# Optimization experiments

Measured on AMD Instinct MI355X. Metric: run time of the kernel, lower is better.

## Reference

```python
import jax, jax.numpy as jnp
import numpy as np

B, O, I, D = 8, 128, 128, 1024


def setup_inputs() -> dict:
    key = jax.random.key(0)
    ks = jax.random.split(key, 10)
    s = 1.0 / np.sqrt(2 * D)  # torch Linear default-ish scale
    return {
        "output": jax.random.normal(ks[0], (B, O, D), jnp.float32),
        "context": jax.random.normal(ks[1], (B, I, D), jnp.float32),
        "mask": jax.random.randint(ks[2], (B, I), 0, 2, jnp.int32),
        # self.w = Linear(2*dim, dim), split into the output-half and context-half
        "w_out_w": jax.random.normal(ks[3], (D, D), jnp.float32) * s,
        "w_ctx_w": jax.random.normal(ks[4], (D, D), jnp.float32) * s,
        "w_b": jax.random.normal(ks[5], (D,), jnp.float32) * s,
        # self.score = Linear(dim, 1)
        "score_w": jax.random.normal(ks[6], (D,), jnp.float32) * (1.0 / np.sqrt(D)),
        "score_b": jnp.zeros((), jnp.float32),
        # self.linear_out = Linear(2*dim, dim)
        "lin_w": jax.random.normal(ks[7], (2 * D, D), jnp.float32) * s,
        "lin_b": jax.random.normal(ks[8], (D,), jnp.float32) * s,
    }


def reference(output, context, mask, w_out_w, w_ctx_w, w_b, score_w, score_b, lin_w, lin_b):
    # Additive (Bahdanau) attention.
    # cat(out, ctx) @ W^T == out @ W1 + ctx @ W2  -> avoid [B,O,I,2D] concat.
    s_out = jnp.einsum('bod,de->boe', output, w_out_w)            # [B,O,D]
    s_ctx = jnp.einsum('bid,de->bie', context, w_ctx_w)           # [B,I,D]
    h = jax.nn.leaky_relu(s_out[:, :, None, :] + s_ctx[:, None, :, :] + w_b)  # [B,O,I,D]
    score = jnp.einsum('boid,d->boi', h, score_w) + score_b       # [B,O,I]
    score = jnp.where(mask[:, None, :] == 1, -jnp.inf, score)
    attn = jax.nn.softmax(score, axis=-1)                         # [B,O,I]
    attn_output = jnp.einsum('boi,bid->bod', attn, context)       # mix=True: bmm
    # fn=True: linear_out on cat(attn_output, output) then leaky_relu
    combined = jnp.concatenate([attn_output, output], axis=-1)    # [B,O,2D]
    attn_output = jax.nn.leaky_relu(combined @ lin_w + lin_b)     # [B,O,D]
    return attn_output, attn
```

## Files before the change

kernel.cpp:

```cpp
#include <hip/hip_runtime.h>

namespace {

constexpr int kB = 8, kO = 128, kI = 128, kD = 1024;
constexpr long kOutAttnOff = (long)kB * kO * kD;

typedef __attribute__((ext_vector_type(8))) short short8;
typedef __attribute__((ext_vector_type(4))) float f32x4;
typedef __attribute__((ext_vector_type(2))) float f32x2;
typedef __attribute__((ext_vector_type(2))) unsigned u32x2;

__device__ __forceinline__ float leaky(float x) { return fmaxf(x, 0.01f * x); }

__device__ __forceinline__ short f2bf(float f) {
    unsigned u = __builtin_bit_cast(unsigned, f);
    u += 0x7FFFu + ((u >> 16) & 1u);
    return (short)(u >> 16);
}
__device__ __forceinline__ float bf2f(short h) {
    return __builtin_bit_cast(float, ((unsigned)(unsigned short)h) << 16);
}
__device__ __forceinline__ void b8tofs(const short8 v, float* f) {
    const unsigned* u = (const unsigned*)&v;
#pragma unroll
    for (int j = 0; j < 4; ++j) {
        f[2 * j]     = __builtin_bit_cast(float, u[j] << 16);
        f[2 * j + 1] = __builtin_bit_cast(float, u[j] & 0xffff0000u);
    }
}
__device__ __forceinline__ void bpair(const short8 a, const short8 b, f32x2* p) {
    float fa[8], fb[8];
    b8tofs(a, fa); b8tofs(b, fb);
#pragma unroll
    for (int j = 0; j < 8; ++j) p[j] = f32x2{fa[j], fb[j]};
}
__device__ __forceinline__ f32x2 vabs2(f32x2 x) {
    u32x2 u = __builtin_bit_cast(u32x2, x);
    u &= 0x7fffffffu;
    return __builtin_bit_cast(f32x2, u);
}

__device__ __forceinline__ void gll16(const void* g, void* l) {
    __builtin_amdgcn_global_load_lds(
        (const __attribute__((address_space(1))) int*)g,
        (__attribute__((address_space(3))) int*)l, 16, 0, 0);
}

__global__ __launch_bounds__(256)
void conv_all(const float* __restrict__ output, const float* __restrict__ context,
              const float* __restrict__ w1, const float* __restrict__ w2,
              const float* __restrict__ lin,
              short* __restrict__ ob16, short* __restrict__ cb16,
              short* __restrict__ w1t, short* __restrict__ w2t,
              short* __restrict__ lint)
{
    __shared__ float T[64][68];
    const int bid = blockIdx.x, tid = threadIdx.x;

    if (bid < 1024) {
        const int idx = bid * 256 + tid;
        const float* src; short* dst; int i;
        if (idx < (1 << 17)) { src = output;  dst = ob16; i = idx; }
        else                 { src = context; dst = cb16; i = idx - (1 << 17); }
        const float4* s4 = (const float4*)src + (long)i * 2;
        const float4 v0 = s4[0], v1 = s4[1];
        short8 r;
        r[0] = f2bf(v0.x); r[1] = f2bf(v0.y); r[2] = f2bf(v0.z); r[3] = f2bf(v0.w);
        r[4] = f2bf(v1.x); r[5] = f2bf(v1.y); r[6] = f2bf(v1.z); r[7] = f2bf(v1.w);
        *(short8*)(dst + (long)i * 8) = r;
        return;
    }

    const int tb = bid - 1024;
    const float* src; short* dst; long C, R; int t2;
    if (tb < 256)      { src = w1;  dst = w1t;  R = 1024; C = 1024; t2 = tb; }
    else if (tb < 512) { src = w2;  dst = w2t;  R = 1024; C = 1024; t2 = tb - 256; }
    else               { src = lin; dst = lint; R = 2048; C = 1024; t2 = tb - 512; }
    const int tr = t2 >> 4, tc = t2 & 15;
    const int r = tid >> 2, q = tid & 3;

    const float* s = src + (long)(tr * 64 + r) * C + tc * 64 + q * 16;
    const float4 a0 = ((const float4*)s)[0];
    const float4 a1 = ((const float4*)s)[1];
    const float4 a2 = ((const float4*)s)[2];
    const float4 a3 = ((const float4*)s)[3];
    *(float4*)&T[r][q * 16 + 0]  = a0;
    *(float4*)&T[r][q * 16 + 4]  = a1;
    *(float4*)&T[r][q * 16 + 8]  = a2;
    *(float4*)&T[r][q * 16 + 12] = a3;
    __syncthreads();

    short8 o0, o1;
#pragma unroll
    for (int j = 0; j < 8; ++j)  o0[j] = f2bf(T[q * 16 + j][r]);
#pragma unroll
    for (int j = 0; j < 8; ++j)  o1[j] = f2bf(T[q * 16 + 8 + j][r]);
    short* dp = dst + (long)(tc * 64 + r) * R + tr * 64 + q * 16;
    *(short8*)dp       = o0;
    *((short8*)dp + 1) = o1;
}

__global__ __launch_bounds__(256)
void mm_jobs(const short* __restrict__ ob16, const short* __restrict__ cb16,
             const short* __restrict__ w1t, const short* __restrict__ w2t,
             const short* __restrict__ lint,
             const float* __restrict__ w_b, const float* __restrict__ lin_b,
             float* __restrict__ s_out, short* __restrict__ s_ctx16,
             float* __restrict__ outlin, short* __restrict__ ctxlin)
{
    __shared__ short As[2][64][64];
    __shared__ short Bs[2][128][64];
    const int tid = threadIdx.x;
    const int t = blockIdx.x;
    const int lane = tid & 63, w = tid >> 6;

    const short *Ap, *Bp;
    int lda, ldb, bm, bn, ldc;
    const float* bias = nullptr;
    float* Cf = nullptr;
    short* Ch = nullptr;

    if (t < 384) {
        const int job = t >> 7, jt = t & 127;
        bm = (jt >> 3) * 64; bn = (jt & 7) * 128;
        lda = 1024; ldc = 1024;
        if (job == 0)      { Ap = ob16; Bp = w1t;         ldb = 1024; bias = w_b;   Cf = s_out;   }
        else if (job == 1) { Ap = cb16; Bp = w2t;         ldb = 1024;               Ch = s_ctx16; }
        else               { Ap = ob16; Bp = lint + 1024; ldb = 2048; bias = lin_b; Cf = outlin;  }
    } else {
        const int tt = t - 384, bz = tt >> 4, tw = tt & 15;
        bm = tw * 64; bn = 0;
        Ap = lint; lda = 2048;
        Bp = cb16 + (long)bz * (kI * kD); ldb = 1024;
        Ch = ctxlin + (long)bz * (kD * kI); ldc = 128;
    }

    const int m0 = (w >> 1) * 32, n0 = (w & 1) * 64;
    const int fr = lane & 15, fcol = lane >> 4, sl = lane & 7;
    const int r8 = lane >> 3;
    const int sw8 = ((lane & 7) ^ r8) * 8;
    const int w16 = w * 16, w32 = w * 32;

    f32x4 acc[2][4] = {};

    auto stage = [&](int buf, int k0) {
        const short* ga = Ap + (long)(bm + w16 + r8) * lda + k0 + sw8;
        gll16(ga,                 &As[buf][w16][0]);
        gll16(ga + 8 * (long)lda, &As[buf][w16 + 8][0]);
        const short* gb = Bp + (long)(bn + w32 + r8) * ldb + k0 + sw8;
        gll16(gb,                  &Bs[buf][w32][0]);
        gll16(gb + 8 * (long)ldb,  &Bs[buf][w32 + 8][0]);
        gll16(gb + 16 * (long)ldb, &Bs[buf][w32 + 16][0]);
        gll16(gb + 24 * (long)ldb, &Bs[buf][w32 + 24][0]);
    };

    stage(0, 0);
    __syncthreads();
    int cur = 0;
    for (int s = 0; s < 16; ++s) {
        if (s < 15) stage(cur ^ 1, (s + 1) << 6);
#pragma unroll
        for (int ks8 = 0; ks8 < 8; ks8 += 4) {
            const int sa = ((ks8 + fcol) ^ sl) * 8;
            short8 a[2], b[4];
#pragma unroll
            for (int mi = 0; mi < 2; ++mi)
                a[mi] = *(const short8*)&As[cur][m0 + mi * 16 + fr][sa];
#pragma unroll
            for (int ni = 0; ni < 4; ++ni)
                b[ni] = *(const short8*)&Bs[cur][n0 + ni * 16 + fr][sa];
#pragma unroll
            for (int mi = 0; mi < 2; ++mi)
#pragma unroll
                for (int ni = 0; ni < 4; ++ni)
                    acc[mi][ni] = __builtin_amdgcn_mfma_f32_16x16x32_bf16(
                        a[mi], b[ni], acc[mi][ni], 0, 0, 0);
        }
        __syncthreads();
        cur ^= 1;
    }

    float bv[4] = {0, 0, 0, 0};
    if (bias) {
#pragma unroll
        for (int ni = 0; ni < 4; ++ni) bv[ni] = bias[bn + n0 + ni * 16 + fr];
    }
#pragma unroll
    for (int mi = 0; mi < 2; ++mi)
#pragma unroll
        for (int ni = 0; ni < 4; ++ni)
#pragma unroll
            for (int r = 0; r < 4; ++r) {
                const int row = bm + m0 + mi * 16 + ((lane >> 4) << 2) + r;
                const int col = bn + n0 + ni * 16 + fr;
                float v = acc[mi][ni][r] + bv[ni];
                if (Ch) Ch[(long)row * ldc + col] = f2bf(v);
                else    Cf[(long)row * ldc + col] = v;
            }
}

__global__ __launch_bounds__(256, 3)
void score_final(const float* __restrict__ s_out, const short* __restrict__ s_ctx16,
                 const float* __restrict__ score_w, const float* __restrict__ score_b,
                 const int* __restrict__ mask, const short* __restrict__ ctxlin,
                 const float* __restrict__ outlin, float* __restrict__ out_main,
                 float* __restrict__ attn_f32)
{
    __shared__ float As[2][1032];
    __shared__ __align__(16) char CsPool[32768];
    __shared__ short Wsh[1032];
    __shared__ float Ps[4][2][128];
    __shared__ float Psi[4][128];
    __shared__ float so_sh[2];
    __shared__ int   Msk[128];
    __shared__ __align__(16) short Pl[16][136];

    short* CsS = (short*)CsPool;
    const int b   = blockIdx.x;
    const int o0  = blockIdx.y * 2;
    const int tid = threadIdx.x;
    const int wv  = tid >> 6;
    const int ln  = tid & 63;
    const int fr  = ln & 15, fg = ln >> 4;

    const short* crow = s_ctx16 + (long)b * kI * kD;
    auto stageCs = [&](int slot, int dc) {
#pragma unroll
        for (int it = 0; it < 4; ++it) {
            const int rb = wv * 32 + it * 8;
            const int r  = rb + (ln >> 3);
            const int sc = (ln & 7) ^ (r & 7);
            gll16(crow + (long)r * kD + dc + sc * 8, CsS + slot * 8192 + rb * 64);
        }
    };

    stageCs(0, 0);

    const float* arow = s_out + (long)(b * kO + o0) * kD;
#pragma unroll
    for (int q = 0; q < 2; ++q) {
        const int tq = tid + q * 256;
        const int rr = tq >> 8, c4 = (tq & 255) * 4;
        *(float4*)&As[rr][c4] = *(const float4*)&arow[(long)rr * kD + c4];
    }
    {
        const float4 w4 = *(const float4*)&score_w[tid * 4];
        const unsigned p0 = (unsigned)(unsigned short)f2bf(w4.x)
                          | ((unsigned)(unsigned short)f2bf(w4.y) << 16);
        const unsigned p1 = (unsigned)(unsigned short)f2bf(w4.z)
                          | ((unsigned)(unsigned short)f2bf(w4.w) << 16);
        *(u32x2*)&Wsh[tid * 4] = u32x2{p0, p1};
    }
    if (tid < 128) Msk[tid] = mask[b * kI + tid];
    {
        short* pf = &Pl[0][0];
        for (int j = tid; j < 272; j += 256) *(short8*)(pf + j * 8) = short8{};
    }
    __syncthreads();

    if (wv < 2) {
        const short8 wA = *(const short8*)&Wsh[ln * 16];
        const short8 wB = *(const short8*)&Wsh[ln * 16 + 8];
        float wf[16];
        b8tofs(wA, wf); b8tofs(wB, wf + 8);
        float acc = 0.0f;
#pragma unroll
        for (int q = 0; q < 4; ++q) {
            const float4 av = *(const float4*)&As[wv][ln * 16 + q * 4];
            acc = fmaf(av.x, wf[q*4+0], acc); acc = fmaf(av.y, wf[q*4+1], acc);
            acc = fmaf(av.z, wf[q*4+2], acc); acc = fmaf(av.w, wf[q*4+3], acc);
        }
#pragma unroll
        for (int d = 1; d < 64; d <<= 1) acc += __shfl_xor(acc, d, 64);
        if (ln == 0) so_sh[wv] = acc;
    }

    f32x2 si2{0.0f, 0.0f};
    f32x2 sa2[2] = {f32x2{0.0f, 0.0f}, f32x2{0.0f, 0.0f}};
    const int kb = wv * 16;

    int buf = 0;
    for (int c = 0; c < 16; ++c) {
        const int dc = c * 64;
        if (c < 15) stageCs(buf ^ 1, dc + 64);
        const short* Cb = CsS + buf * 8192;
        const int sc0 = ((wv * 2 + 0) ^ (ln & 7)) * 8;
        const int sc1 = ((wv * 2 + 1) ^ (ln & 7)) * 8;
        const short8 cA0 = *(const short8*)&Cb[ln * 64 + sc0];
        const short8 cA1 = *(const short8*)&Cb[ln * 64 + sc1];
        const short8 cB0 = *(const short8*)&Cb[(ln + 64) * 64 + sc0];
        const short8 cB1 = *(const short8*)&Cb[(ln + 64) * 64 + sc1];
        f32x2 c2[16];
        bpair(cA0, cB0, c2);
        bpair(cA1, cB1, c2 + 8);
        const short8 w0 = *(const short8*)&Wsh[dc + kb];
        const short8 w1 = *(const short8*)&Wsh[dc + kb + 8];
        float wr[16];
        b8tofs(w0, wr); b8tofs(w1, wr + 8);
        float av0[16], av1[16];
#pragma unroll
        for (int q = 0; q < 4; ++q) {
            *(float4*)&av0[q * 4] = *(const float4*)&As[0][dc + kb + q * 4];
            *(float4*)&av1[q * 4] = *(const float4*)&As[1][dc + kb + q * 4];
        }
#pragma unroll
        for (int d = 0; d < 16; ++d) {
            const f32x2 w2 = {wr[d], wr[d]};
            si2 += c2[d] * w2;
            const f32x2 x0 = c2[d] + f32x2{av0[d], av0[d]};
            const f32x2 x1 = c2[d] + f32x2{av1[d], av1[d]};
            sa2[0] += vabs2(x0) * w2;
            sa2[1] += vabs2(x1) * w2;
        }
        __syncthreads();
        buf ^= 1;
    }

    short* Bsh = (short*)CsPool;
    const short* ctxb = ctxlin + (long)b * (kD * kI);
    auto stageB = [&](int half, int nc) {
#pragma unroll
        for (int it = 0; it < 4; ++it) {
            const int rb = wv * 16 + it * 4;
            const int r  = rb + (ln >> 4);
            const int n  = nc * 64 + r;
            const int sc = (ln & 15) ^ (r & 7);
            gll16(ctxb + (long)n * kI + sc * 8, Bsh + half * 8192 + rb * kI);
        }
    };
    stageB(0, 0);

#pragma unroll
    for (int o = 0; o < 2; ++o) {
        Ps[wv][o][ln]      = sa2[o].x;
        Ps[wv][o][ln + 64] = sa2[o].y;
    }
    Psi[wv][ln]      = si2.x;
    Psi[wv][ln + 64] = si2.y;
    __syncthreads();

    if (wv < 2) {
        const int ow = wv;
        const float negInf = -__builtin_huge_valf();
        const float sb = score_b[0];
        const float siT0 = Psi[0][ln] + Psi[1][ln] + Psi[2][ln] + Psi[3][ln];
        const float siT1 = Psi[0][ln + 64] + Psi[1][ln + 64]
                         + Psi[2][ln + 64] + Psi[3][ln + 64];
        const float saT0 = Ps[0][ow][ln] + Ps[1][ow][ln]
                         + Ps[2][ow][ln] + Ps[3][ow][ln];
        const float saT1 = Ps[0][ow][ln + 64] + Ps[1][ow][ln + 64]
                         + Ps[2][ow][ln + 64] + Ps[3][ow][ln + 64];
        const float soV = so_sh[ow];
        float s0 = 0.505f * (soV + siT0) + 0.495f * saT0 + sb;
        float s1 = 0.505f * (soV + siT1) + 0.495f * saT1 + sb;
        if (Msk[ln]      != 0) s0 = negInf;
        if (Msk[ln + 64] != 0) s1 = negInf;

        float m = fmaxf(s0, s1);
#pragma unroll
        for (int d = 1; d < 64; d <<= 1) m = fmaxf(m, __shfl_xor(m, d, 64));
        const float e0 = __expf(s0 - m);
        const float e1 = __expf(s1 - m);
        float sum = e0 + e1;
#pragma unroll
        for (int d = 1; d < 64; d <<= 1) sum += __shfl_xor(sum, d, 64);
        const float inv = 1.0f / sum;

        const long rowoff = (long)(b * kO + o0 + ow) * kI;
        const float p0 = e0 * inv, p1 = e1 * inv;
        attn_f32[rowoff + ln]      = p0;
        attn_f32[rowoff + ln + 64] = p1;
        Pl[ow][ln]      = f2bf(p0);
        Pl[ow][ln + 64] = f2bf(p1);
    }
    __syncthreads();

    int half = 0;
    for (int nc = 0; nc < 16; ++nc) {
        if (nc < 15) stageB(half ^ 1, nc + 1);
        const short* Bc = Bsh + half * 8192;
        f32x4 acc{};
#pragma unroll
        for (int ks = 0; ks < 4; ++ks) {
            const short8 a = *(const short8*)&Pl[fr][ks * 32 + fg * 8];
            const int sc = ((ks * 4 + fg) ^ (fr & 7)) * 8;
            const short8 bb = *(const short8*)&Bc[(wv * 16 + fr) * kI + sc];
            acc = __builtin_amdgcn_mfma_f32_16x16x32_bf16(a, bb, acc, 0, 0, 0);
        }
        if (fg == 0) {
#pragma unroll
            for (int r = 0; r < 2; ++r) {
                const int n = nc * 64 + wv * 16 + fr;
                const long off = (long)(b * kO + o0 + r) * kD + n;
                out_main[off] = leaky(acc[r] + outlin[off]);
            }
        }
        __syncthreads();
        half ^= 1;
    }
}

}

extern "C" void kernel_launch(void* const* d_in, const int* in_sizes, int n_in,
                              void* d_out, int out_size, void* d_ws, size_t ws_size,
                              hipStream_t stream)
{
    const float* output  = (const float*)d_in[0];
    const float* context = (const float*)d_in[1];
    const int*   mask    = (const int*)d_in[2];
    const float* w_out_w = (const float*)d_in[3];
    const float* w_ctx_w = (const float*)d_in[4];
    const float* w_b     = (const float*)d_in[5];
    const float* score_w = (const float*)d_in[6];
    const float* score_b = (const float*)d_in[7];
    const float* lin_w   = (const float*)d_in[8];
    const float* lin_b   = (const float*)d_in[9];

    float* out_main = (float*)d_out;
    float* out_attn = out_main + kOutAttnOff;
    float* s_out    = out_main;

    char* wp = (char*)d_ws;
    short* s_ctx16 = (short*)wp;  wp += (size_t)2 << 20;
    short* ob16    = (short*)wp;  wp += (size_t)2 << 20;
    short* cb16    = (short*)wp;  wp += (size_t)2 << 20;
    short* w1t     = (short*)wp;  wp += (size_t)2 << 20;
    short* w2t     = (short*)wp;  wp += (size_t)2 << 20;
    short* lint    = (short*)wp;  wp += (size_t)4 << 20;
    float* outlin  = (float*)wp;  wp += (size_t)4 << 20;
    short* ctxlin  = (short*)wp;

    const dim3 blk(256);

    hipLaunchKernelGGL(conv_all, dim3(2048), blk, 0, stream,
        output, context, w_out_w, w_ctx_w, lin_w, ob16, cb16, w1t, w2t, lint);

    hipLaunchKernelGGL(mm_jobs, dim3(512), blk, 0, stream,
        ob16, cb16, w1t, w2t, lint, w_b, lin_b, s_out, s_ctx16, outlin, ctxlin);

    hipLaunchKernelGGL(score_final, dim3(8, 64), blk, 0, stream,
        s_out, s_ctx16, score_w, score_b, mask, ctxlin, outlin, out_main, out_attn);
}
```

Measured before the change: 63.39 us.

## Fuse fp32-to-bf16 activation conversion into GEMM loads and share A tiles

```diff
diff --git a/kernel.cpp b/kernel.cpp
--- a/kernel.cpp
+++ b/kernel.cpp
@@ -17,9 +17,6 @@
     u += 0x7FFFu + ((u >> 16) & 1u);
     return (short)(u >> 16);
 }
-__device__ __forceinline__ float bf2f(short h) {
-    return __builtin_bit_cast(float, ((unsigned)(unsigned short)h) << 16);
-}
 __device__ __forceinline__ void b8tofs(const short8 v, float* f) {
     const unsigned* u = (const unsigned*)&v;
 #pragma unroll
@@ -39,6 +36,12 @@
     u &= 0x7fffffffu;
     return __builtin_bit_cast(f32x2, u);
 }
+__device__ __forceinline__ short8 pack8(const float4 a, const float4 b) {
+    short8 r;
+    r[0] = f2bf(a.x); r[1] = f2bf(a.y); r[2] = f2bf(a.z); r[3] = f2bf(a.w);
+    r[4] = f2bf(b.x); r[5] = f2bf(b.y); r[6] = f2bf(b.z); r[7] = f2bf(b.w);
+    return r;
+}
 
 __device__ __forceinline__ void gll16(const void* g, void* l) {
     __builtin_amdgcn_global_load_lds(
@@ -47,31 +50,14 @@
 }
 
 __global__ __launch_bounds__(256)
-void conv_all(const float* __restrict__ output, const float* __restrict__ context,
-              const float* __restrict__ w1, const float* __restrict__ w2,
-              const float* __restrict__ lin,
-              short* __restrict__ ob16, short* __restrict__ cb16,
-              short* __restrict__ w1t, short* __restrict__ w2t,
-              short* __restrict__ lint)
+void conv_t(const float* __restrict__ w1, const float* __restrict__ w2,
+            const float* __restrict__ lin,
+            short* __restrict__ w1t, short* __restrict__ w2t,
+            short* __restrict__ lint)
 {
     __shared__ float T[64][68];
-    const int bid = blockIdx.x, tid = threadIdx.x;
-
-    if (bid < 1024) {
-        const int idx = bid * 256 + tid;
-        const float* src; short* dst; int i;
-        if (idx < (1 << 17)) { src = output;  dst = ob16; i = idx; }
-        else                 { src = context; dst = cb16; i = idx - (1 << 17); }
-        const float4* s4 = (const float4*)src + (long)i * 2;
-        const float4 v0 = s4[0], v1 = s4[1];
-        short8 r;
-        r[0] = f2bf(v0.x); r[1] = f2bf(v0.y); r[2] = f2bf(v0.z); r[3] = f2bf(v0.w);
-        r[4] = f2bf(v1.x); r[5] = f2bf(v1.y); r[6] = f2bf(v1.z); r[7] = f2bf(v1.w);
-        *(short8*)(dst + (long)i * 8) = r;
-        return;
-    }
-
-    const int tb = bid - 1024;
+    const int tb = blockIdx.x, tid = threadIdx.x;
+
     const float* src; short* dst; long C, R; int t2;
     if (tb < 256)      { src = w1;  dst = w1t;  R = 1024; C = 1024; t2 = tb; }
     else if (tb < 512) { src = w2;  dst = w2t;  R = 1024; C = 1024; t2 = tb - 256; }
@@ -100,65 +86,128 @@
     *((short8*)dp + 1) = o1;
 }
 
-__global__ __launch_bounds__(256)
-void mm_jobs(const short* __restrict__ ob16, const short* __restrict__ cb16,
-             const short* __restrict__ w1t, const short* __restrict__ w2t,
-             const short* __restrict__ lint,
-             const float* __restrict__ w_b, const float* __restrict__ lin_b,
-             float* __restrict__ s_out, short* __restrict__ s_ctx16,
-             float* __restrict__ outlin, short* __restrict__ ctxlin)
+__global__ __launch_bounds__(256, 3)
+void mm_jobs2(const float* __restrict__ output, const float* __restrict__ context,
+              const short* __restrict__ w1t, const short* __restrict__ w2t,
+              const short* __restrict__ lint,
+              const float* __restrict__ w_b, const float* __restrict__ lin_b,
+              float* __restrict__ s_out, short* __restrict__ s_ctx16,
+              float* __restrict__ outlin, short* __restrict__ ctxlin)
 {
     __shared__ short As[2][64][64];
     __shared__ short Bs[2][128][64];
+
     const int tid = threadIdx.x;
-    const int t = blockIdx.x;
+    const int t = (blockIdx.x & 7) * 64 + (blockIdx.x >> 3);
     const int lane = tid & 63, w = tid >> 6;
-
-    const short *Ap, *Bp;
-    int lda, ldb, bm, bn, ldc;
-    const float* bias = nullptr;
-    float* Cf = nullptr;
-    short* Ch = nullptr;
-
-    if (t < 384) {
-        const int job = t >> 7, jt = t & 127;
-        bm = (jt >> 3) * 64; bn = (jt & 7) * 128;
-        lda = 1024; ldc = 1024;
-        if (job == 0)      { Ap = ob16; Bp = w1t;         ldb = 1024; bias = w_b;   Cf = s_out;   }
-        else if (job == 1) { Ap = cb16; Bp = w2t;         ldb = 1024;               Ch = s_ctx16; }
-        else               { Ap = ob16; Bp = lint + 1024; ldb = 2048; bias = lin_b; Cf = outlin;  }
+    const int r8 = lane >> 3, c8 = lane & 7;
+    const int sw8 = (c8 ^ r8) * 8;
+    const int w16 = w * 16;
+
+    const float* Afp = nullptr;
+    const short* Abf = nullptr;
+    const float* Bfp = nullptr;
+    const short *Bb0 = nullptr, *Bb1 = nullptr;
+    long ldb0 = 1024, ldb1 = 1024;
+    int brow0 = 0, brow1 = 0, bko0 = 0, bko1 = 0;
+    float* Cfh[2] = {nullptr, nullptr};
+    short* Chh[2] = {nullptr, nullptr};
+    const float* bias[2] = {nullptr, nullptr};
+    int colbase[2] = {0, 0}, ldc = 1024, bm;
+
+    if (t < 256) {
+        bm = (t & 15) * 64; const int bn = (t >> 4) * 64;
+        Afp = output;
+        Bb0 = w1t;  brow0 = bn; ldb0 = 1024; bko0 = 0;
+        Bb1 = lint; brow1 = bn; ldb1 = 2048; bko1 = 1024;
+        Cfh[0] = s_out; Cfh[1] = outlin;
+        bias[0] = w_b;  bias[1] = lin_b;
+        colbase[0] = bn; colbase[1] = bn;
+    } else if (t < 384) {
+        const int tl = t - 256;
+        bm = (tl & 15) * 64; const int bnp = (tl >> 4) * 128;
+        Afp = context;
+        Bb0 = w2t; brow0 = bnp;      ldb0 = 1024; bko0 = 0;
+        Bb1 = w2t; brow1 = bnp + 64; ldb1 = 1024; bko1 = 0;
+        Chh[0] = s_ctx16; Chh[1] = s_ctx16;
+        colbase[0] = bnp; colbase[1] = bnp + 64;
     } else {
-        const int tt = t - 384, bz = tt >> 4, tw = tt & 15;
-        bm = tw * 64; bn = 0;
-        Ap = lint; lda = 2048;
-        Bp = cb16 + (long)bz * (kI * kD); ldb = 1024;
-        Ch = ctxlin + (long)bz * (kD * kI); ldc = 128;
-    }
+        const int tl = t - 384;
+        bm = (tl & 15) * 64; const int bz = tl >> 4;
+        Abf = lint;
+        Bfp = context + (long)bz * (kI * kD);
+        short* c = ctxlin + (long)bz * (kD * kI);
+        Chh[0] = c; Chh[1] = c;
+        colbase[0] = 0; colbase[1] = 64; ldc = 128;
+    }
+
+    float4 av4[4], bv4[8];
+    auto loadA = [&](int k0) {
+        const float* g = Afp + (long)(bm + w16 + r8) * 1024 + k0 + sw8;
+        av4[0] = ((const float4*)g)[0];
+        av4[1] = ((const float4*)g)[1];
+        const float* g2 = g + 8 * 1024;
+        av4[2] = ((const float4*)g2)[0];
+        av4[3] = ((const float4*)g2)[1];
+    };
+    auto writeA = [&](int buf) {
+        *(short8*)&As[buf][w16 + r8][c8 * 8]     = pack8(av4[0], av4[1]);
+        *(short8*)&As[buf][w16 + 8 + r8][c8 * 8] = pack8(av4[2], av4[3]);
+    };
+    auto stageAbf = [&](int buf, int k0) {
+        const short* ga = Abf + (long)(bm + w16 + r8) * 2048 + k0 + sw8;
+        gll16(ga,            &As[buf][w16][0]);
+        gll16(ga + 8 * 2048, &As[buf][w16 + 8][0]);
+    };
+    auto stageBbf = [&](int buf, int k0) {
+        const short* src = (w < 2) ? Bb0 : Bb1;
+        const long  ldb  = (w < 2) ? ldb0 : ldb1;
+        const int   br   = ((w < 2) ? brow0 : brow1) + (w & 1) * 32;
+        const int   ko   = (w < 2) ? bko0 : bko1;
+        const short* gb = src + (long)(br + r8) * ldb + k0 + ko + sw8;
+        gll16(gb,            &Bs[buf][w * 32][0]);
+        gll16(gb + 8 * ldb,  &Bs[buf][w * 32 + 8][0]);
+        gll16(gb + 16 * ldb, &Bs[buf][w * 32 + 16][0]);
+        gll16(gb + 24 * ldb, &Bs[buf][w * 32 + 24][0]);
+    };
+    auto loadB = [&](int k0) {
+        const float* g = Bfp + (long)(w16 + r8) * 1024 + k0 + sw8;
+        bv4[0] = ((const float4*)g)[0];
+        bv4[1] = ((const float4*)g)[1];
+        const float* g2 = g + 8 * 1024;
+        bv4[2] = ((const float4*)g2)[0];
+        bv4[3] = ((const float4*)g2)[1];
+        const float* gh = g + 64 * 1024;
+        bv4[4] = ((const float4*)gh)[0];
+        bv4[5] = ((const float4*)gh)[1];
+        const float* gh2 = gh + 8 * 1024;
+        bv4[6] = ((const float4*)gh2)[0];
+        bv4[7] = ((const float4*)gh2)[1];
+    };
+    auto writeB = [&](int buf) {
+        *(short8*)&Bs[buf][w16 + r8][c8 * 8]          = pack8(bv4[0], bv4[1]);
+        *(short8*)&Bs[buf][w16 + 8 + r8][c8 * 8]      = pack8(bv4[2], bv4[3]);
+        *(short8*)&Bs[buf][64 + w16 + r8][c8 * 8]     = pack8(bv4[4], bv4[5]);
+        *(short8*)&Bs[buf][64 + w16 + 8 + r8][c8 * 8] = pack8(bv4[6], bv4[7]);
+    };
 
     const int m0 = (w >> 1) * 32, n0 = (w & 1) * 64;
     const int fr = lane & 15, fcol = lane >> 4, sl = lane & 7;
-    const int r8 = lane >> 3;
-    const int sw8 = ((lane & 7) ^ r8) * 8;
-    const int w16 = w * 16, w32 = w * 32;
-
     f32x4 acc[2][4] = {};
 
-    auto stage = [&](int buf, int k0) {
-        const short* ga = Ap + (long)(bm + w16 + r8) * lda + k0 + sw8;
-        gll16(ga,                 &As[buf][w16][0]);
-        gll16(ga + 8 * (long)lda, &As[buf][w16 + 8][0]);
-        const short* gb = Bp + (long)(bn + w32 + r8) * ldb + k0 + sw8;
-        gll16(gb,                  &Bs[buf][w32][0]);
-        gll16(gb + 8 * (long)ldb,  &Bs[buf][w32 + 8][0]);
-        gll16(gb + 16 * (long)ldb, &Bs[buf][w32 + 16][0]);
-        gll16(gb + 24 * (long)ldb, &Bs[buf][w32 + 24][0]);
-    };
-
-    stage(0, 0);
+    if (Afp) loadA(0); else stageAbf(0, 0);
+    if (Bfp) loadB(0); else stageBbf(0, 0);
+    if (Afp) writeA(0);
+    if (Bfp) writeB(0);
     __syncthreads();
+
     int cur = 0;
     for (int s = 0; s < 16; ++s) {
-        if (s < 15) stage(cur ^ 1, (s + 1) << 6);
+        const int nxt = cur ^ 1;
+        if (s < 15) {
+            if (Afp) loadA((s + 1) << 6); else stageAbf(nxt, (s + 1) << 6);
+            if (Bfp) loadB((s + 1) << 6); else stageBbf(nxt, (s + 1) << 6);
+        }
 #pragma unroll
         for (int ks8 = 0; ks8 < 8; ks8 += 4) {
             const int sa = ((ks8 + fcol) ^ sl) * 8;
@@ -176,14 +225,19 @@
                     acc[mi][ni] = __builtin_amdgcn_mfma_f32_16x16x32_bf16(
                         a[mi], b[ni], acc[mi][ni], 0, 0, 0);
         }
-        __syncthreads();
-        cur ^= 1;
-    }
-
+        if (s < 15) {
+            if (Afp) writeA(nxt);
+            if (Bfp) writeB(nxt);
+            __syncthreads();
+        }
+        cur = nxt;
+    }
+
+    const int h = w & 1;
     float bv[4] = {0, 0, 0, 0};
-    if (bias) {
-#pragma unroll
-        for (int ni = 0; ni < 4; ++ni) bv[ni] = bias[bn + n0 + ni * 16 + fr];
+    if (bias[h]) {
+#pragma unroll
+        for (int ni = 0; ni < 4; ++ni) bv[ni] = bias[h][colbase[h] + ni * 16 + fr];
     }
 #pragma unroll
     for (int mi = 0; mi < 2; ++mi)
@@ -192,10 +246,10 @@
 #pragma unroll
             for (int r = 0; r < 4; ++r) {
                 const int row = bm + m0 + mi * 16 + ((lane >> 4) << 2) + r;
-                const int col = bn + n0 + ni * 16 + fr;
-                float v = acc[mi][ni][r] + bv[ni];
-                if (Ch) Ch[(long)row * ldc + col] = f2bf(v);
-                else    Cf[(long)row * ldc + col] = v;
+                const int col = colbase[h] + ni * 16 + fr;
+                const float v = acc[mi][ni][r] + bv[ni];
+                if (Chh[h]) Chh[h][(long)row * ldc + col] = f2bf(v);
+                else        Cfh[h][(long)row * ldc + col] = v;
             }
 }
 
@@ -423,21 +477,20 @@
 
     char* wp = (char*)d_ws;
     short* s_ctx16 = (short*)wp;  wp += (size_t)2 << 20;
-    short* ob16    = (short*)wp;  wp += (size_t)2 << 20;
-    short* cb16    = (short*)wp;  wp += (size_t)2 << 20;
+    float* outlin  = (float*)wp;  wp += (size_t)4 << 20;
+    short* ctxlin  = (short*)wp;  wp += (size_t)2 << 20;
     short* w1t     = (short*)wp;  wp += (size_t)2 << 20;
     short* w2t     = (short*)wp;  wp += (size_t)2 << 20;
-    short* lint    = (short*)wp;  wp += (size_t)4 << 20;
-    float* outlin  = (float*)wp;  wp += (size_t)4 << 20;
-    short* ctxlin  = (short*)wp;
+    short* lint    = (short*)wp;
 
     const dim3 blk(256);
 
-    hipLaunchKernelGGL(conv_all, dim3(2048), blk, 0, stream,
-        output, context, w_out_w, w_ctx_w, lin_w, ob16, cb16, w1t, w2t, lint);
-
-    hipLaunchKernelGGL(mm_jobs, dim3(512), blk, 0, stream,
-        ob16, cb16, w1t, w2t, lint, w_b, lin_b, s_out, s_ctx16, outlin, ctxlin);
+    hipLaunchKernelGGL(conv_t, dim3(1024), blk, 0, stream,
+        w_out_w, w_ctx_w, lin_w, w1t, w2t, lint);
+
+    hipLaunchKernelGGL(mm_jobs2, dim3(512), blk, 0, stream,
+        output, context, w1t, w2t, lint, w_b, lin_b,
+        s_out, s_ctx16, outlin, ctxlin);
 
     hipLaunchKernelGGL(score_final, dim3(8, 64), blk, 0, stream,
         s_out, s_ctx16, score_w, score_b, mask, ctxlin, outlin, out_main, out_attn);
```

New measurement: 67.46 us. 6.4% more time.
